# Optimization experiments

Hardware: AMD Instinct MI355X
Metric: run time of the kernel (lower is better)

The kernel has to match this reference:

```python
import jax, jax.numpy as jnp
import numpy as np

N = 100000   # nodes
E = 400000   # merged window edges
L = 100000   # label edges to decode
DIN = 128
H = 128
NL = 2       # GCN layers
RATIO = 0.8
DOUT = 1


def setup_inputs() -> dict:
    key = jax.random.key(0)
    ks = jax.random.split(key, 24)
    def nrm(k, shape, fan):
        return (jax.random.normal(k, shape, jnp.float32) / np.sqrt(fan)).astype(jnp.float32)
    inp = {
        'x': jax.random.normal(ks[0], (N, DIN), jnp.float32),
        'edge_index': jax.random.randint(ks[1], (2, E), 0, N, jnp.int64) if jax.config.jax_enable_x64 else jax.random.randint(ks[1], (2, E), 0, N, jnp.int32),
        'edge_label_index': jax.random.randint(ks[2], (2, L), 0, N, jnp.int32),
        'edge_time': jax.random.uniform(ks[3], (E,), jnp.float32),
        'previous_state': jax.random.normal(ks[4], (N, H), jnp.float32),
        # mlp_transform: Linear(DIN,H)+ReLU
        'w_mlp': nrm(ks[5], (DIN, H), DIN), 'b_mlp': jnp.zeros((H,), jnp.float32),
        # TimeEncode: cos(Linear(1,H)(t))
        'w_time': nrm(ks[6], (H,), 1), 'b_time': jnp.zeros((H,), jnp.float32),
        # Sampling MLP: Linear(3H,H)+ReLU, Linear(H,1)
        'w_s1': nrm(ks[7], (3 * H, H), 3 * H), 'b_s1': jnp.zeros((H,), jnp.float32),
        'w_s2': nrm(ks[8], (H, 1), H), 'b_s2': jnp.zeros((1,), jnp.float32),
        # GCNConv weights per layer
        'gcn_w': nrm(ks[9], (NL, H, H), H), 'gcn_b': jnp.zeros((NL, H), jnp.float32),
        # GRUCell (stored as [H,3H] so x @ W is the torch x @ W_ih^T)
        'gru_wi': nrm(ks[10], (H, 3 * H), H), 'gru_wh': nrm(ks[11], (H, 3 * H), H),
        'gru_bi': jnp.zeros((3 * H,), jnp.float32), 'gru_bh': jnp.zeros((3 * H,), jnp.float32),
        # LinkDecoder: (h_src * h_dst) @ W + b
        'w_dec': nrm(ks[12], (H, DOUT), H), 'b_dec': jnp.zeros((DOUT,), jnp.float32),
    }
    return inp


def _gcn_pass(h, s2, d2, norm, W, b):
    m = h @ W                                      # [N,H]
    agg = jax.ops.segment_sum(norm[:, None] * m[s2], d2, num_segments=N)
    return agg + b


def reference(x, edge_index, edge_label_index, edge_time, previous_state,
              w_mlp, b_mlp, w_time, b_time, w_s1, b_s1, w_s2, b_s2,
              gcn_w, gcn_b, gru_wi, gru_wh, gru_bi, gru_bh, w_dec, b_dec):
    h = jax.nn.relu(x @ w_mlp + b_mlp)             # [N,H]
    src, dst = edge_index[0], edge_index[1]
    # time encoding of shifted edge times: cos(t*w + b) -> [E,H]
    t = edge_time - edge_time.min() + 1.0
    te = jnp.cos(t[:, None] * w_time + b_time)
    # Sampling logits; concat(prev[src],prev[dst],te) @ w_s1 done as 3 matmuls
    pre = (previous_state[src] @ w_s1[:H] + previous_state[dst] @ w_s1[H:2 * H]
           + te @ w_s1[2 * H:] + b_s1)
    logits = jax.nn.relu(pre) @ w_s2 + b_s2        # [E,1]
    z = jax.nn.sigmoid(logits[:, 0])               # eval mode: no Gumbel noise
    k = int(RATIO * E)
    _, keep = jax.lax.top_k(z, k)
    ew, s, d = z[keep], src[keep], dst[keep]
    # GCN normalization with self-loops (weight 1), symmetric norm as in PyG
    sl = jnp.arange(N, dtype=s.dtype)
    s2 = jnp.concatenate([s, sl]); d2 = jnp.concatenate([d, sl])
    w2 = jnp.concatenate([ew, jnp.ones((N,), ew.dtype)])
    deg = jax.ops.segment_sum(w2, d2, num_segments=N)
    dinv = jnp.where(deg > 0, jax.lax.rsqrt(deg), 0.0)
    norm = dinv[s2] * w2 * dinv[d2]                # [k+N]
    for i in range(NL):
        h = _gcn_pass(h, s2, d2, norm, gcn_w[i], gcn_b[i])
        if i != NL - 1:
            h = jax.nn.relu(h)
    # GRUCell update (torch semantics)
    gi = h @ gru_wi + gru_bi
    gh = previous_state @ gru_wh + gru_bh
    ir, iz, inn = jnp.split(gi, 3, axis=1)
    hr, hz, hn = jnp.split(gh, 3, axis=1)
    r = jax.nn.sigmoid(ir + hr)
    u = jax.nn.sigmoid(iz + hz)
    n = jnp.tanh(inn + r * hn)
    h_new = (1.0 - u) * n + u * previous_state     # [N,H]
    # LinkDecoder: Hadamard of endpoints -> linear
    pred = (h_new[edge_label_index[0]] * h_new[edge_label_index[1]]) @ w_dec + b_dec
    return pred, h_new
```

## Files before the change

kernel.cpp:

```cpp
#include <hip/hip_runtime.h>
#include <hip/hip_bf16.h>
#include <math.h>

typedef __bf16 bf16_t;
typedef bf16_t bf16x8 __attribute__((ext_vector_type(8)));
typedef bf16_t bf16x2 __attribute__((ext_vector_type(2)));
typedef float  f32x4  __attribute__((ext_vector_type(4)));
typedef float  f32x2  __attribute__((ext_vector_type(2)));

__device__ __forceinline__ int clampi(int v, int n) {
    return v < 0 ? 0 : (v > n - 1 ? n - 1 : v);
}

template<int NC>
__global__ __launch_bounds__(256) void gemm128(const bf16_t* __restrict__ A,
        const bf16_t* __restrict__ BT, const float* __restrict__ bias,
        float* __restrict__ Cf, bf16_t* __restrict__ Cb, int M, int dorelu)
{
    constexpr int NT = NC / 16;
    int wave = threadIdx.x >> 6, lane = threadIdx.x & 63;
    int mbase = (blockIdx.x * 4 + wave) * 16;
    if (mbase >= M) return;
    int r = lane & 15, q = lane >> 4;
    int arow = mbase + r; if (arow > M - 1) arow = M - 1;
    f32x4 acc[NT];
#pragma unroll
    for (int t = 0; t < NT; ++t) acc[t] = f32x4{0.f, 0.f, 0.f, 0.f};
    const bf16_t* aptr = A + (size_t)arow * 128 + q * 8;
#pragma unroll
    for (int kk = 0; kk < 4; ++kk) {
        bf16x8 af = *(const bf16x8*)(aptr + kk * 32);
#pragma unroll
        for (int t = 0; t < NT; ++t) {
            bf16x8 bfg = *(const bf16x8*)(BT + (size_t)(t * 16 + r) * 128 + kk * 32 + q * 8);
            acc[t] = __builtin_amdgcn_mfma_f32_16x16x32_bf16(af, bfg, acc[t], 0, 0, 0);
        }
    }
#pragma unroll
    for (int t = 0; t < NT; ++t) {
#pragma unroll
        for (int i = 0; i < 4; ++i) {
            int row = mbase + q * 4 + i;
            if (row < M) {
                int col = t * 16 + r;
                float v = acc[t][i];
                if (bias) v += bias[col];
                if (dorelu) v = fmaxf(v, 0.f);
                if (Cf) Cf[(size_t)row * NC + col] = v;
                if (Cb) Cb[(size_t)row * NC + col] = (bf16_t)v;
            }
        }
    }
}

__global__ __launch_bounds__(256) void gru_k(const bf16_t* __restrict__ xb,
        const float* __restrict__ prevf, const bf16_t* __restrict__ wiT,
        const bf16_t* __restrict__ whT, const float* __restrict__ bi,
        const float* __restrict__ bh, float* __restrict__ hnew, int M)
{
    int wave = threadIdx.x >> 6, lane = threadIdx.x & 63;
    int mbase = (blockIdx.x * 4 + wave) * 16;
    if (mbase >= M) return;
    int r = lane & 15, q = lane >> 4;
    int arow = mbase + r; if (arow > M - 1) arow = M - 1;
    bf16x8 ax[4], ap[4];
#pragma unroll
    for (int kk = 0; kk < 4; ++kk) {
        ax[kk] = *(const bf16x8*)(xb + (size_t)arow * 128 + kk * 32 + q * 8);
        f32x4 p0 = *(const f32x4*)(prevf + (size_t)arow * 128 + kk * 32 + q * 8);
        f32x4 p1 = *(const f32x4*)(prevf + (size_t)arow * 128 + kk * 32 + q * 8 + 4);
        bf16x8 t;
#pragma unroll
        for (int j = 0; j < 4; ++j) { t[j] = (bf16_t)p0[j]; t[j + 4] = (bf16_t)p1[j]; }
        ap[kk] = t;
    }
#pragma unroll
    for (int t3 = 0; t3 < 8; ++t3) {
        f32x4 gi0{0.f,0.f,0.f,0.f}, gi1{0.f,0.f,0.f,0.f}, gi2{0.f,0.f,0.f,0.f};
        f32x4 gh0{0.f,0.f,0.f,0.f}, gh1{0.f,0.f,0.f,0.f}, gh2{0.f,0.f,0.f,0.f};
#pragma unroll
        for (int kk = 0; kk < 4; ++kk) {
            const bf16_t* wi = wiT + (size_t)(t3 * 16 + r) * 128 + kk * 32 + q * 8;
            const bf16_t* wh = whT + (size_t)(t3 * 16 + r) * 128 + kk * 32 + q * 8;
            gi0 = __builtin_amdgcn_mfma_f32_16x16x32_bf16(ax[kk], *(const bf16x8*)wi, gi0, 0, 0, 0);
            gi1 = __builtin_amdgcn_mfma_f32_16x16x32_bf16(ax[kk], *(const bf16x8*)(wi + 128 * 128), gi1, 0, 0, 0);
            gi2 = __builtin_amdgcn_mfma_f32_16x16x32_bf16(ax[kk], *(const bf16x8*)(wi + 256 * 128), gi2, 0, 0, 0);
            gh0 = __builtin_amdgcn_mfma_f32_16x16x32_bf16(ap[kk], *(const bf16x8*)wh, gh0, 0, 0, 0);
            gh1 = __builtin_amdgcn_mfma_f32_16x16x32_bf16(ap[kk], *(const bf16x8*)(wh + 128 * 128), gh1, 0, 0, 0);
            gh2 = __builtin_amdgcn_mfma_f32_16x16x32_bf16(ap[kk], *(const bf16x8*)(wh + 256 * 128), gh2, 0, 0, 0);
        }
        int f = t3 * 16 + r;
        float bif0 = bi[f], bif1 = bi[128 + f], bif2 = bi[256 + f];
        float bhf0 = bh[f], bhf1 = bh[128 + f], bhf2 = bh[256 + f];
#pragma unroll
        for (int i = 0; i < 4; ++i) {
            int row = mbase + q * 4 + i;
            if (row < M) {
                float ir = gi0[i] + bif0, hr = gh0[i] + bhf0;
                float iz = gi1[i] + bif1, hz = gh1[i] + bhf1;
                float inn = gi2[i] + bif2, hn = gh2[i] + bhf2;
                float rg = 1.f / (1.f + expf(-(ir + hr)));
                float ug = 1.f / (1.f + expf(-(iz + hz)));
                float nn = tanhf(inn + rg * hn);
                float hp = prevf[(size_t)row * 128 + f];
                hnew[(size_t)row * 128 + f] = (1.f - ug) * nn + ug * hp;
            }
        }
    }
}

__global__ void transp_k(const float* __restrict__ src, bf16_t* __restrict__ dst,
                         int cols, int ld, int rowoff)
{
    int i = blockIdx.x * blockDim.x + threadIdx.x;
    if (i >= cols * 128) return;
    int n = i >> 7, kk = i & 127;
    dst[i] = (bf16_t)src[(size_t)(rowoff + kk) * ld + n];
}

__global__ void cvtb_k(const float* __restrict__ src, size_t off0,
                       bf16_t* __restrict__ dst, int n)
{
    for (int i = blockIdx.x * blockDim.x + threadIdx.x; i < n; i += gridDim.x * blockDim.x)
        dst[i] = (bf16_t)src[off0 + (size_t)i];
}

__global__ void init_k(unsigned* meta, float* deg, int N, int k)
{
    int i = blockIdx.x * blockDim.x + threadIdx.x;
    if (i == 0) { meta[0] = 0x7f800000u; meta[1] = (unsigned)k; meta[8] = 0u; }
    if (i < N) deg[i] = 1.0f;
}

__global__ void tmin_k(const float* __restrict__ et, unsigned* meta, int E)
{
    __shared__ float sred[4];
    int i = blockIdx.x * blockDim.x + threadIdx.x;
    int stride = gridDim.x * blockDim.x;
    float v = 1e30f;
    for (; i < E; i += stride) v = fminf(v, et[i]);
    for (int off = 32; off; off >>= 1) v = fminf(v, __shfl_down(v, off, 64));
    int wave = threadIdx.x >> 6, lane = threadIdx.x & 63;
    if (lane == 0) sred[wave] = v;
    __syncthreads();
    if (threadIdx.x == 0) {
        v = fminf(fminf(sred[0], sred[1]), fminf(sred[2], sred[3]));
        atomicMin(meta + 0, __float_as_uint(v));
    }
}

__global__ void bcount_k(const int* __restrict__ ei, unsigned* bmeta, int E, int Nh, int N)
{
    __shared__ unsigned sc[4];
    int tid = threadIdx.x;
    if (tid < 4) sc[tid] = 0;
    __syncthreads();
    int e = blockIdx.x * blockDim.x + tid;
    int b = -1;
    if (e < E) {
        int s = clampi(ei[e], N), d = clampi(ei[E + e], N);
        b = (s >= Nh ? 2 : 0) + (d >= Nh ? 1 : 0);
    }
    int lane = tid & 63;
#pragma unroll
    for (int bb = 0; bb < 4; ++bb) {
        unsigned long long m = __ballot(b == bb);
        if (lane == 0 && m) atomicAdd(sc + bb, (unsigned)__popcll(m));
    }
    __syncthreads();
    if (tid < 4 && sc[tid]) atomicAdd(bmeta + tid, sc[tid]);
}

__global__ void bscan_k(unsigned* bmeta)
{
    if (threadIdx.x == 0 && blockIdx.x == 0) {
        bmeta[4] = 0;
        for (int b = 0; b < 4; ++b) {
            bmeta[5 + b] = bmeta[4 + b] + bmeta[b];
            bmeta[9 + b] = bmeta[4 + b];
        }
    }
}

__global__ void bfill_k(const int* __restrict__ ei, unsigned* bmeta,
                        unsigned* __restrict__ elist, int E, int Nh, int N)
{
    __shared__ unsigned scount[4];
    __shared__ unsigned sbase[4];
    int tid = threadIdx.x;
    if (tid < 4) scount[tid] = 0;
    __syncthreads();
    int e = blockIdx.x * blockDim.x + tid;
    int b = -1;
    if (e < E) {
        int s = clampi(ei[e], N), d = clampi(ei[E + e], N);
        b = (s >= Nh ? 2 : 0) + (d >= Nh ? 1 : 0);
    }
    int lane = tid & 63;
    unsigned myofs = 0;
#pragma unroll
    for (int bb = 0; bb < 4; ++bb) {
        unsigned long long m = __ballot(b == bb);
        unsigned wb = 0;
        if (lane == 0 && m) wb = atomicAdd(scount + bb, (unsigned)__popcll(m));
        wb = __shfl(wb, 0, 64);
        if (b == bb) myofs = wb + (unsigned)__popcll(m & ((1ull << lane) - 1ull));
    }
    __syncthreads();
    if (tid < 4) sbase[tid] = scount[tid] ? atomicAdd(bmeta + 9 + tid, scount[tid]) : 0u;
    __syncthreads();
    if (b >= 0) elist[sbase[b] + myofs] = (unsigned)e;
}

__global__ __launch_bounds__(256, 2) void proj2(const float* __restrict__ prevf,
        const float* __restrict__ Wflat, float* __restrict__ out, int rows, int base)
{
    __shared__ float sA[16][132];
    __shared__ float sB[16][128];
    int tid = threadIdx.x;
    int rbase = blockIdx.x * 128;
    if (rbase >= rows) return;
    int tx = tid & 15, ty = tid >> 4;
    float acc[8][8];
#pragma unroll
    for (int i = 0; i < 8; ++i)
#pragma unroll
        for (int j = 0; j < 8; ++j) acc[i][j] = 0.f;
    int ks = tid & 15, rs = tid >> 4;
    int fs = tid & 127, kbs = tid >> 7;
    for (int kc = 0; kc < 128; kc += 16) {
#pragma unroll
        for (int i = 0; i < 8; ++i) {
            int r = rs + 16 * i;
            int rr = rbase + r; if (rr > rows - 1) rr = rows - 1;
            sA[ks][r] = prevf[(size_t)(base + rr) * 128 + kc + ks];
        }
#pragma unroll
        for (int i = 0; i < 8; ++i)
            sB[kbs + 2 * i][fs] = Wflat[(size_t)(kc + kbs + 2 * i) * 128 + fs];
        __syncthreads();
#pragma unroll
        for (int r = 0; r < 16; ++r) {
            f32x4 a0 = *(const f32x4*)&sA[r][ty * 8];
            f32x4 a1 = *(const f32x4*)&sA[r][ty * 8 + 4];
            f32x4 b0 = *(const f32x4*)&sB[r][tx * 4];
            f32x4 b1 = *(const f32x4*)&sB[r][64 + tx * 4];
#pragma unroll
            for (int i = 0; i < 8; ++i) {
                float ae = i < 4 ? a0[i] : a1[i - 4];
#pragma unroll
                for (int j = 0; j < 4; ++j) {
                    acc[i][j]     = fmaf(ae, b0[j], acc[i][j]);
                    acc[i][j + 4] = fmaf(ae, b1[j], acc[i][j + 4]);
                }
            }
        }
        __syncthreads();
    }
#pragma unroll
    for (int i = 0; i < 8; ++i) {
        int row = rbase + ty * 8 + i;
        if (row < rows) {
            f32x4 o0, o1;
#pragma unroll
            for (int j = 0; j < 4; ++j) { o0[j] = acc[i][j]; o1[j] = acc[i][j + 4]; }
            *(f32x4*)&out[(size_t)row * 128 + tx * 4] = o0;
            *(f32x4*)&out[(size_t)row * 128 + 64 + tx * 4] = o1;
        }
    }
}

__global__ __launch_bounds__(256, 2) void zgemm(
        const float* __restrict__ et, const int* __restrict__ ei,
        const unsigned* __restrict__ elist, const unsigned* __restrict__ bmeta, int b,
        int soff, int doff,
        const float* __restrict__ Ah, const float* __restrict__ Bh,
        const float* __restrict__ wtime, const float* __restrict__ btime,
        const float* __restrict__ wc, const float* __restrict__ bs1,
        const float* __restrict__ ws2, const float* __restrict__ bs2,
        const unsigned* __restrict__ meta,
        float* __restrict__ z, unsigned* __restrict__ hist1, int E, int N)
{
    unsigned lo = 0, hi = (unsigned)E;
    if (b >= 0) { lo = bmeta[4 + b]; hi = bmeta[5 + b]; }
    unsigned ebase = (unsigned)blockIdx.x * 128u;
    if (ebase >= hi - lo) return;
    __shared__ float sA[16][132];
    __shared__ float sB[16][128];
    __shared__ float sT[128];
    __shared__ int sS[128], sD[128];
    __shared__ unsigned sE[128];
    int tid = threadIdx.x;
    if (tid < 128) {
        float tmin = __uint_as_float(meta[0]);
        unsigned slot = lo + ebase + (unsigned)tid;
        unsigned sl = slot < hi ? slot : hi - 1u;
        unsigned e = elist ? elist[sl] : sl;
        sE[tid] = e;
        sT[tid] = et[e] - tmin + 1.0f;
        sS[tid] = clampi(ei[e], N) - soff;
        sD[tid] = clampi(ei[E + e], N) - doff;
    }
    __syncthreads();
    int tx = tid & 15, ty = tid >> 4;
    float acc[8][8];
#pragma unroll
    for (int i = 0; i < 8; ++i)
#pragma unroll
        for (int j = 0; j < 8; ++j) acc[i][j] = 0.f;
    int ks = tid & 15, rs = tid >> 4;
    int fs = tid & 127, kbs = tid >> 7;
    for (int kc = 0; kc < 128; kc += 16) {
        float wt = wtime[kc + ks], bt = btime[kc + ks];
#pragma unroll
        for (int i = 0; i < 8; ++i) {
            float t = sT[rs + 16 * i];
            sA[ks][rs + 16 * i] = cosf(t * wt + bt);
        }
#pragma unroll
        for (int i = 0; i < 8; ++i)
            sB[kbs + 2 * i][fs] = wc[(size_t)(kc + kbs + 2 * i) * 128 + fs];
        __syncthreads();
#pragma unroll
        for (int r = 0; r < 16; ++r) {
            f32x4 a0 = *(const f32x4*)&sA[r][ty * 8];
            f32x4 a1 = *(const f32x4*)&sA[r][ty * 8 + 4];
            f32x4 b0 = *(const f32x4*)&sB[r][tx * 4];
            f32x4 b1 = *(const f32x4*)&sB[r][64 + tx * 4];
#pragma unroll
            for (int i = 0; i < 8; ++i) {
                float ae = i < 4 ? a0[i] : a1[i - 4];
#pragma unroll
                for (int j = 0; j < 4; ++j) {
                    acc[i][j]     = fmaf(ae, b0[j], acc[i][j]);
                    acc[i][j + 4] = fmaf(ae, b1[j], acc[i][j + 4]);
                }
            }
        }
        __syncthreads();
    }
    f32x4 bb0 = *(const f32x4*)&bs1[tx * 4];
    f32x4 bb1 = *(const f32x4*)&bs1[64 + tx * 4];
    f32x4 w20 = *(const f32x4*)&ws2[tx * 4];
    f32x4 w21 = *(const f32x4*)&ws2[64 + tx * 4];
    float myv = 0.f;
#pragma unroll
    for (int i = 0; i < 8; ++i) {
        int r = ty * 8 + i;
        int s = sS[r], d = sD[r];
        const float* As = Ah + (size_t)s * 128;
        const float* Bd = Bh + (size_t)d * 128;
        f32x4 A0 = *(const f32x4*)&As[tx * 4];
        f32x4 A1 = *(const f32x4*)&As[64 + tx * 4];
        f32x4 B0 = *(const f32x4*)&Bd[tx * 4];
        f32x4 B1 = *(const f32x4*)&Bd[64 + tx * 4];
        float v[4];
#pragma unroll
        for (int j = 0; j < 4; ++j) {
            float p0 = acc[i][j] + ((A0[j] + B0[j]) + bb0[j]);
            float p1 = acc[i][j + 4] + ((A1[j] + B1[j]) + bb1[j]);
            v[j] = fmaxf(p0, 0.f) * w20[j] + fmaxf(p1, 0.f) * w21[j];
        }
#pragma unroll
        for (int j = 0; j < 4; ++j) {
            v[j] += __shfl_xor(v[j], 8, 64);
            v[j] += __shfl_xor(v[j], 4, 64);
            v[j] += __shfl_xor(v[j], 2, 64);
            v[j] += __shfl_xor(v[j], 1, 64);
        }
        float vv = (v[0] + v[2]) + (v[1] + v[3]);
        if (tx == i) myv = vv;
    }
    if (tx < 8) {
        int r = ty * 8 + tx;
        unsigned slot = lo + ebase + (unsigned)r;
        if (slot < hi) {
            float b2 = bs2[0];
            float zv = 1.f / (1.f + expf(-(myv + b2)));
            z[sE[r]] = zv;
            atomicAdd(hist1 + (__float_as_uint(zv) >> 16), 1u);
        }
    }
}

__global__ __launch_bounds__(1024) void scank(const unsigned* __restrict__ hist,
                                              unsigned* meta, int kIdx, int outIdx)
{
    __shared__ unsigned s[1024];
    int t = threadIdx.x;
    unsigned K = meta[kIdx];
    unsigned sum = 0;
    for (int i = 0; i < 64; ++i) sum += hist[t * 64 + i];
    s[t] = sum;
    __syncthreads();
    for (int off = 1; off < 1024; off <<= 1) {
        unsigned add = (t + off < 1024) ? s[t + off] : 0u;
        __syncthreads();
        s[t] += add;
        __syncthreads();
    }
    unsigned mine = s[t];
    unsigned after = (t < 1023) ? s[t + 1] : 0u;
    if (mine >= K && after < K) {
        unsigned cum = after;
        for (int b = 63; b >= 0; --b) {
            unsigned c = hist[t * 64 + b];
            cum += c;
            if (cum >= K) {
                meta[outIdx] = (unsigned)(t * 64 + b);
                meta[outIdx + 1] = cum - c;
                meta[outIdx + 2] = K - (cum - c);
                break;
            }
        }
    }
}

__global__ void pass2(const float* __restrict__ z, const unsigned* __restrict__ meta,
                      unsigned* hist2, int E)
{
    int e = blockIdx.x * blockDim.x + threadIdx.x;
    if (e >= E) return;
    unsigned u = __float_as_uint(z[e]);
    if ((u >> 16) == meta[2]) atomicAdd(hist2 + (u & 0xffffu), 1u);
}

__global__ void pass3(const float* __restrict__ z, unsigned* meta,
                      unsigned char* keep, unsigned* eql, int E)
{
    int e = blockIdx.x * blockDim.x + threadIdx.x;
    if (e >= E) return;
    unsigned u = __float_as_uint(z[e]);
    unsigned T = (meta[2] << 16) | (meta[5] & 0xffffu);
    keep[e] = (u > T) ? 1 : 0;
    if (u == T) {
        unsigned slot = atomicAdd(meta + 8, 1u);
        if (slot < 4096u) eql[slot] = (unsigned)e;
    }
}

__global__ void eqres(const unsigned* __restrict__ meta, const unsigned* __restrict__ eql,
                      unsigned char* keep)
{
    __shared__ unsigned list[4096];
    unsigned c = meta[8]; if (c > 4096u) c = 4096u;
    unsigned need = meta[7];
    for (unsigned i = threadIdx.x; i < c; i += blockDim.x) list[i] = eql[i];
    __syncthreads();
    for (unsigned i = threadIdx.x; i < c; i += blockDim.x) {
        unsigned rank = 0;
        for (unsigned j = 0; j < c; ++j) rank += (list[j] < list[i]) ? 1u : 0u;
        if (rank < need) keep[list[i]] = 1;
    }
}

__global__ void degsc(const int* __restrict__ ei, const float* __restrict__ z,
                      const unsigned char* __restrict__ keep, float* deg, int E, int N)
{
    int e = blockIdx.x * blockDim.x + threadIdx.x;
    if (e >= E) return;
    if (keep[e]) atomicAdd(deg + clampi(ei[E + e], N), z[e]);
}

__global__ void dinv_k(float* deg, float* selfn, int N)
{
    int i = blockIdx.x * blockDim.x + threadIdx.x;
    if (i >= N) return;
    float d = deg[i];
    float di = 1.0f / sqrtf(d);
    deg[i] = di;
    selfn[i] = di * di;
}

__global__ void normcnt(const int* __restrict__ ei, const float* __restrict__ z,
                        const unsigned char* __restrict__ keep, const float* __restrict__ dinv,
                        float* normv, unsigned* cnt, int E, int N)
{
    int e = blockIdx.x * blockDim.x + threadIdx.x;
    if (e >= E) return;
    if (keep[e]) {
        int s = clampi(ei[e], N), d = clampi(ei[E + e], N);
        normv[e] = dinv[s] * z[e] * dinv[d];
        atomicAdd(cnt + d, 1u);
    } else {
        normv[e] = 0.f;
    }
}

__global__ __launch_bounds__(1024) void scan_n(unsigned* cnt, unsigned* fill, int N)
{
    __shared__ unsigned s[1024];
    int t = threadIdx.x;
    int per = (N + 1023) >> 10;
    int lo = t * per; if (lo > N) lo = N;
    int hi = lo + per; if (hi > N) hi = N;
    unsigned sum = 0;
    for (int i = lo; i < hi; ++i) sum += cnt[i];
    s[t] = sum;
    __syncthreads();
    for (int off = 1; off < 1024; off <<= 1) {
        unsigned add = (t >= off) ? s[t - off] : 0u;
        __syncthreads();
        s[t] += add;
        __syncthreads();
    }
    unsigned run = (t > 0) ? s[t - 1] : 0u;
    for (int i = lo; i < hi; ++i) {
        unsigned c = cnt[i];
        cnt[i] = run; fill[i] = run;
        run += c;
    }
    if (t == 1023) cnt[N] = run;
}

__global__ void fillk(const int* __restrict__ ei, const unsigned char* __restrict__ keep,
                      unsigned* fill, unsigned* csr, int E, int N)
{
    int e = blockIdx.x * blockDim.x + threadIdx.x;
    if (e >= E) return;
    if (keep[e]) {
        unsigned p = atomicAdd(fill + clampi(ei[E + e], N), 1u);
        csr[p] = (unsigned)e;
    }
}

__global__ __launch_bounds__(256) void agg_k(const bf16_t* __restrict__ m,
        const int* __restrict__ ei, const float* __restrict__ normv,
        const unsigned* __restrict__ ofs, const unsigned* __restrict__ csr,
        const float* __restrict__ selfn, const float* __restrict__ bias,
        float* __restrict__ hout, bf16_t* __restrict__ houtb, int N, int E, int dorelu)
{
    int wave = threadIdx.x >> 6, lane = threadIdx.x & 63;
    int n = blockIdx.x * 4 + wave;
    if (n >= N) return;
    int f = 2 * lane;
    float sn = selfn[n];
    bf16x2 mv = *(const bf16x2*)(m + (size_t)n * 128 + f);
    float a0 = bias[f] + sn * (float)mv[0];
    float a1 = bias[f + 1] + sn * (float)mv[1];
    unsigned lo = ofs[n], hi = ofs[n + 1];
    unsigned deg = hi - lo;
    unsigned cap = deg < 64u ? deg : 64u;
    int s_l = 0; float w_l = 0.f;
    if (lane < (int)cap) {
        unsigned e = csr[lo + lane];
        s_l = clampi(ei[e], N);
        w_l = normv[e];
    }
    for (unsigned j = 0; j < cap; ++j) {
        int s = __shfl(s_l, (int)j, 64);
        float w = __shfl(w_l, (int)j, 64);
        bf16x2 v = *(const bf16x2*)(m + (size_t)s * 128 + f);
        a0 = fmaf(w, (float)v[0], a0);
        a1 = fmaf(w, (float)v[1], a1);
    }
    for (unsigned idx = lo + 64; idx < hi; ++idx) {
        unsigned e = csr[idx];
        int s = clampi(ei[e], N);
        float w = normv[e];
        bf16x2 v = *(const bf16x2*)(m + (size_t)s * 128 + f);
        a0 = fmaf(w, (float)v[0], a0);
        a1 = fmaf(w, (float)v[1], a1);
    }
    if (dorelu) { a0 = fmaxf(a0, 0.f); a1 = fmaxf(a1, 0.f); }
    f32x2 o; o[0] = a0; o[1] = a1;
    *(f32x2*)(hout + (size_t)n * 128 + f) = o;
    if (houtb) {
        bf16x2 ob; ob[0] = (bf16_t)a0; ob[1] = (bf16_t)a1;
        *(bf16x2*)(houtb + (size_t)n * 128 + f) = ob;
    }
}

__global__ __launch_bounds__(256) void decode_k(const int* __restrict__ eli,
        const float* __restrict__ hnew, const float* __restrict__ wdec,
        const float* __restrict__ bdec, float* __restrict__ pred, int L, int N)
{
    int wave = threadIdx.x >> 6, lane = threadIdx.x & 63;
    int l = blockIdx.x * 4 + wave;
    if (l >= L) return;
    int a = clampi(eli[l], N), b = clampi(eli[L + l], N);
    f32x2 ha = *(const f32x2*)(hnew + (size_t)a * 128 + 2 * lane);
    f32x2 hb = *(const f32x2*)(hnew + (size_t)b * 128 + 2 * lane);
    f32x2 w  = *(const f32x2*)(wdec + 2 * lane);
    float acc = ha[0] * hb[0] * w[0] + ha[1] * hb[1] * w[1];
    for (int off = 32; off; off >>= 1) acc += __shfl_down(acc, off, 64);
    if (lane == 0) pred[l] = acc + bdec[0];
}

extern "C" void kernel_launch(void* const* d_in, const int* in_sizes, int n_in,
                              void* d_out, int out_size, void* d_ws, size_t ws_size,
                              hipStream_t stream)
{
    (void)n_in; (void)out_size;
    const float* x      = (const float*)d_in[0];
    const int*   ei     = (const int*)d_in[1];
    const int*   eli    = (const int*)d_in[2];
    const float* etime  = (const float*)d_in[3];
    const float* prev   = (const float*)d_in[4];
    const float* w_mlp  = (const float*)d_in[5];
    const float* b_mlp  = (const float*)d_in[6];
    const float* w_time = (const float*)d_in[7];
    const float* b_time = (const float*)d_in[8];
    const float* w_s1   = (const float*)d_in[9];
    const float* b_s1   = (const float*)d_in[10];
    const float* w_s2   = (const float*)d_in[11];
    const float* b_s2   = (const float*)d_in[12];
    const float* gcn_w  = (const float*)d_in[13];
    const float* gcn_b  = (const float*)d_in[14];
    const float* gru_wi = (const float*)d_in[15];
    const float* gru_wh = (const float*)d_in[16];
    const float* gru_bi = (const float*)d_in[17];
    const float* gru_bh = (const float*)d_in[18];
    const float* w_dec  = (const float*)d_in[19];
    const float* b_dec  = (const float*)d_in[20];

    const int E  = in_sizes[3];
    const int N  = in_sizes[0] / 128;
    const int L  = in_sizes[2] / 2;
    const int K  = (int)(0.8 * (double)E);
    const int Nh = (N + 1) / 2;

    char* wsp = (char*)d_ws;
    size_t off = 0;
    auto alloc = [&](size_t bytes) -> void* {
        void* p = wsp + off;
        off += (bytes + 255) & ~(size_t)255;
        return p;
    };
    unsigned* meta  = (unsigned*)alloc(64 * 4);
    unsigned* bmeta = (unsigned*)alloc(64 * 4);
    unsigned* elist = (unsigned*)alloc((size_t)E * 4);
    unsigned* eql   = (unsigned*)alloc(4096 * 4);
    unsigned* hist1 = (unsigned*)alloc(65536 * 4);
    unsigned* hist2 = (unsigned*)alloc(65536 * 4);
    unsigned* cnt   = (unsigned*)alloc((size_t)(N + 1) * 4);
    unsigned* fill  = (unsigned*)alloc((size_t)N * 4);
    float* deg      = (float*)alloc((size_t)N * 4);
    float* selfn    = (float*)alloc((size_t)N * 4);
    float* zbuf     = (float*)alloc((size_t)E * 4);
    unsigned char* keep = (unsigned char*)alloc((size_t)E);
    float* normv    = (float*)alloc((size_t)E * 4);
    unsigned* csr   = (unsigned*)alloc((size_t)E * 4);
    bf16_t* wmlpT = (bf16_t*)alloc(128 * 128 * 2);
    bf16_t* g0T   = (bf16_t*)alloc(128 * 128 * 2);
    bf16_t* g1T   = (bf16_t*)alloc(128 * 128 * 2);
    bf16_t* wiT   = (bf16_t*)alloc(384 * 128 * 2);
    bf16_t* whT   = (bf16_t*)alloc(384 * 128 * 2);

    size_t fullBytes = (size_t)N * 128 * 4;
    size_t halfBytes = (size_t)Nh * 128 * 4;
    bool full = (off + 2 * ((fullBytes + 255) & ~(size_t)255)) <= ws_size;
    char* slot0; char* slot1;
    float* Ahalf; float* Bhalf;
    if (full) {
        slot0 = (char*)alloc(fullBytes);
        slot1 = (char*)alloc(fullBytes);
        Ahalf = (float*)slot0;
        Bhalf = (float*)slot1;
    } else {
        slot0 = (char*)alloc(halfBytes);
        slot1 = (char*)alloc(halfBytes);
        Ahalf = (float*)slot0;
        Bhalf = (float*)slot1;
    }
    bf16_t* xbf   = (bf16_t*)slot0;
    bf16_t* mbuf  = (bf16_t*)slot1;

    float* out_pred = (float*)d_out;
    float* hnew     = (float*)d_out + L;
    float* hb       = hnew;

    hipMemsetAsync(bmeta, 0, 64 * 4, stream);
    hipMemsetAsync(hist1, 0, 65536 * 4, stream);
    hipMemsetAsync(hist2, 0, 65536 * 4, stream);
    hipMemsetAsync(cnt, 0, (size_t)(N + 1) * 4, stream);
    init_k<<<(N + 255) / 256, 256, 0, stream>>>(meta, deg, N, K);

    transp_k<<<64, 256, 0, stream>>>(w_mlp, wmlpT, 128, 128, 0);
    transp_k<<<64, 256, 0, stream>>>(gcn_w, g0T, 128, 128, 0);
    transp_k<<<64, 256, 0, stream>>>(gcn_w, g1T, 128, 128, 128);
    transp_k<<<192, 256, 0, stream>>>(gru_wi, wiT, 384, 384, 0);
    transp_k<<<192, 256, 0, stream>>>(gru_wh, whT, 384, 384, 0);

    tmin_k<<<512, 256, 0, stream>>>(etime, meta, E);

    const int zgrid = (E + 127) / 128;
    const float* wc = w_s1 + 256 * 128;
    if (full) {
        proj2<<<(N + 127) / 128, 256, 0, stream>>>(prev, w_s1, Ahalf, N, 0);
        proj2<<<(N + 127) / 128, 256, 0, stream>>>(prev, w_s1 + 128 * 128, Bhalf, N, 0);
        zgemm<<<zgrid, 256, 0, stream>>>(etime, ei, (const unsigned*)nullptr, bmeta, -1,
                0, 0, Ahalf, Bhalf, w_time, b_time, wc, b_s1, w_s2, b_s2,
                meta, zbuf, hist1, E, N);
    } else {
        bcount_k<<<(E + 255) / 256, 256, 0, stream>>>(ei, bmeta, E, Nh, N);
        bscan_k<<<1, 64, 0, stream>>>(bmeta);
        bfill_k<<<(E + 255) / 256, 256, 0, stream>>>(ei, bmeta, elist, E, Nh, N);
        const int NA0 = Nh, NA1 = N - Nh;
        auto zlaunch = [&](int b, int so, int doo) {
            zgemm<<<zgrid, 256, 0, stream>>>(etime, ei, elist, bmeta, b, so, doo,
                    Ahalf, Bhalf, w_time, b_time, wc, b_s1, w_s2, b_s2,
                    meta, zbuf, hist1, E, N);
        };
        proj2<<<(NA0 + 127) / 128, 256, 0, stream>>>(prev, w_s1, Ahalf, NA0, 0);
        proj2<<<(NA0 + 127) / 128, 256, 0, stream>>>(prev, w_s1 + 128 * 128, Bhalf, NA0, 0);
        zlaunch(0, 0, 0);
        proj2<<<(NA1 + 127) / 128, 256, 0, stream>>>(prev, w_s1 + 128 * 128, Bhalf, NA1, Nh);
        zlaunch(1, 0, Nh);
        proj2<<<(NA1 + 127) / 128, 256, 0, stream>>>(prev, w_s1, Ahalf, NA1, Nh);
        zlaunch(3, Nh, Nh);
        proj2<<<(NA0 + 127) / 128, 256, 0, stream>>>(prev, w_s1 + 128 * 128, Bhalf, NA0, 0);
        zlaunch(2, Nh, 0);
    }

    scank<<<1, 1024, 0, stream>>>(hist1, meta, 1, 2);
    pass2<<<(E + 255) / 256, 256, 0, stream>>>(zbuf, meta, hist2, E);
    scank<<<1, 1024, 0, stream>>>(hist2, meta, 4, 5);
    pass3<<<(E + 255) / 256, 256, 0, stream>>>(zbuf, meta, keep, eql, E);
    eqres<<<1, 256, 0, stream>>>(meta, eql, keep);

    degsc<<<(E + 255) / 256, 256, 0, stream>>>(ei, zbuf, keep, deg, E, N);
    dinv_k<<<(N + 255) / 256, 256, 0, stream>>>(deg, selfn, N);
    normcnt<<<(E + 255) / 256, 256, 0, stream>>>(ei, zbuf, keep, deg, normv, cnt, E, N);
    scan_n<<<1, 1024, 0, stream>>>(cnt, fill, N);
    fillk<<<(E + 255) / 256, 256, 0, stream>>>(ei, keep, fill, csr, E, N);

    cvtb_k<<<2048, 256, 0, stream>>>(x, 0, xbf, N * 128);
    gemm128<128><<<(N + 63) / 64, 256, 0, stream>>>(xbf, wmlpT, b_mlp, hb, xbf, N, 1);

    gemm128<128><<<(N + 63) / 64, 256, 0, stream>>>(xbf, g0T, nullptr, nullptr, mbuf, N, 0);
    agg_k<<<(N + 3) / 4, 256, 0, stream>>>(mbuf, ei, normv, cnt, csr, selfn, gcn_b, hb, xbf, N, E, 1);
    gemm128<128><<<(N + 63) / 64, 256, 0, stream>>>(xbf, g1T, nullptr, nullptr, mbuf, N, 0);
    agg_k<<<(N + 3) / 4, 256, 0, stream>>>(mbuf, ei, normv, cnt, csr, selfn, gcn_b + 128, hb, xbf, N, E, 0);

    gru_k<<<(N + 63) / 64, 256, 0, stream>>>(xbf, prev, wiT, whT, gru_bi, gru_bh, hnew, N);

    decode_k<<<(L + 3) / 4, 256, 0, stream>>>(eli, hnew, w_dec, b_dec, out_pred, L, N);
}
```

Baseline: 1.517 ms.

## Make projection and z GEMMs wave-independent and fuse init memsets into one kernel

The proj2 and zgemm kernels are restructured so each wave handles its own 32 rows or edges, with a per-wave LDS tile and no block-wide barriers. The weight operand is now read straight from global or L2 instead of being staged in shared memory. Launch bounds go up to 4 blocks per CU for more occupancy. The four memsets plus init kernel become one grid-stride init kernel, removing launch overhead. The risk is more redundant global weight reads per wave, and relying on compiler-only fences for intra-wave LDS ordering.

Result: slower. 1.669 ms (+10.1%).

```diff
diff --git a/kernel.cpp b/kernel.cpp
--- a/kernel.cpp
+++ b/kernel.cpp
@@ -125,11 +125,16 @@
         dst[i] = (bf16_t)src[off0 + (size_t)i];
 }
 
-__global__ void init_k(unsigned* meta, float* deg, int N, int k)
+__global__ void initall(unsigned* meta, unsigned* bmeta, unsigned* hist1,
+                        unsigned* hist2, unsigned* cnt, float* deg, int N, int k)
 {
     int i = blockIdx.x * blockDim.x + threadIdx.x;
+    int stride = gridDim.x * blockDim.x;
     if (i == 0) { meta[0] = 0x7f800000u; meta[1] = (unsigned)k; meta[8] = 0u; }
-    if (i < N) deg[i] = 1.0f;
+    if (i < 64) bmeta[i] = 0u;
+    for (int j = i; j < 65536; j += stride) { hist1[j] = 0u; hist2[j] = 0u; }
+    for (int j = i; j < N + 1; j += stride) cnt[j] = 0u;
+    for (int j = i; j < N; j += stride) deg[j] = 1.0f;
 }
 
 __global__ void tmin_k(const float* __restrict__ et, unsigned* meta, int E)
@@ -212,39 +217,36 @@
     if (b >= 0) elist[sbase[b] + myofs] = (unsigned)e;
 }
 
-__global__ __launch_bounds__(256, 2) void proj2(const float* __restrict__ prevf,
+__global__ __launch_bounds__(256, 4) void proj2w(const float* __restrict__ prevf,
         const float* __restrict__ Wflat, float* __restrict__ out, int rows, int base)
 {
-    __shared__ float sA[16][132];
-    __shared__ float sB[16][128];
-    int tid = threadIdx.x;
-    int rbase = blockIdx.x * 128;
+    __shared__ float sP[4][16][36];
+    int wave = threadIdx.x >> 6, lane = threadIdx.x & 63;
+    int rbase = blockIdx.x * 128 + wave * 32;
     if (rbase >= rows) return;
-    int tx = tid & 15, ty = tid >> 4;
+    int tx = lane & 15, eg = lane >> 4;
+    int kk = lane & 15, e0 = (lane >> 4) * 8;
     float acc[8][8];
 #pragma unroll
     for (int i = 0; i < 8; ++i)
 #pragma unroll
         for (int j = 0; j < 8; ++j) acc[i][j] = 0.f;
-    int ks = tid & 15, rs = tid >> 4;
-    int fs = tid & 127, kbs = tid >> 7;
     for (int kc = 0; kc < 128; kc += 16) {
+        float tmp[8];
 #pragma unroll
         for (int i = 0; i < 8; ++i) {
-            int r = rs + 16 * i;
-            int rr = rbase + r; if (rr > rows - 1) rr = rows - 1;
-            sA[ks][r] = prevf[(size_t)(base + rr) * 128 + kc + ks];
-        }
-#pragma unroll
-        for (int i = 0; i < 8; ++i)
-            sB[kbs + 2 * i][fs] = Wflat[(size_t)(kc + kbs + 2 * i) * 128 + fs];
-        __syncthreads();
+            int rr = rbase + e0 + i; if (rr > rows - 1) rr = rows - 1;
+            tmp[i] = prevf[(size_t)(base + rr) * 128 + kc + kk];
+        }
+#pragma unroll
+        for (int i = 0; i < 8; ++i) sP[wave][kk][e0 + i] = tmp[i];
+        asm volatile("" ::: "memory");
 #pragma unroll
         for (int r = 0; r < 16; ++r) {
-            f32x4 a0 = *(const f32x4*)&sA[r][ty * 8];
-            f32x4 a1 = *(const f32x4*)&sA[r][ty * 8 + 4];
-            f32x4 b0 = *(const f32x4*)&sB[r][tx * 4];
-            f32x4 b1 = *(const f32x4*)&sB[r][64 + tx * 4];
+            f32x4 a0 = *(const f32x4*)&sP[wave][r][eg * 8];
+            f32x4 a1 = *(const f32x4*)&sP[wave][r][eg * 8 + 4];
+            f32x4 b0 = *(const f32x4*)&Wflat[(size_t)(kc + r) * 128 + tx * 4];
+            f32x4 b1 = *(const f32x4*)&Wflat[(size_t)(kc + r) * 128 + 64 + tx * 4];
 #pragma unroll
             for (int i = 0; i < 8; ++i) {
                 float ae = i < 4 ? a0[i] : a1[i - 4];
@@ -255,11 +257,11 @@
                 }
             }
         }
-        __syncthreads();
+        asm volatile("" ::: "memory");
     }
 #pragma unroll
     for (int i = 0; i < 8; ++i) {
-        int row = rbase + ty * 8 + i;
+        int row = rbase + eg * 8 + i;
         if (row < rows) {
             f32x4 o0, o1;
 #pragma unroll
@@ -270,7 +272,7 @@
     }
 }
 
-__global__ __launch_bounds__(256, 2) void zgemm(
+__global__ __launch_bounds__(256, 4) void zgemmw(
         const float* __restrict__ et, const int* __restrict__ ei,
         const unsigned* __restrict__ elist, const unsigned* __restrict__ bmeta, int b,
         int soff, int doff,
@@ -283,50 +285,48 @@
 {
     unsigned lo = 0, hi = (unsigned)E;
     if (b >= 0) { lo = bmeta[4 + b]; hi = bmeta[5 + b]; }
-    unsigned ebase = (unsigned)blockIdx.x * 128u;
+    int wave = threadIdx.x >> 6, lane = threadIdx.x & 63;
+    unsigned ebase = (unsigned)blockIdx.x * 128u + (unsigned)wave * 32u;
     if (ebase >= hi - lo) return;
-    __shared__ float sA[16][132];
-    __shared__ float sB[16][128];
-    __shared__ float sT[128];
-    __shared__ int sS[128], sD[128];
-    __shared__ unsigned sE[128];
-    int tid = threadIdx.x;
-    if (tid < 128) {
+    __shared__ float sT[4][32];
+    __shared__ int sS[4][32], sD[4][32];
+    __shared__ unsigned sE[4][32];
+    __shared__ float sC[4][16][36];
+    if (lane < 32) {
         float tmin = __uint_as_float(meta[0]);
-        unsigned slot = lo + ebase + (unsigned)tid;
+        unsigned slot = lo + ebase + (unsigned)lane;
         unsigned sl = slot < hi ? slot : hi - 1u;
         unsigned e = elist ? elist[sl] : sl;
-        sE[tid] = e;
-        sT[tid] = et[e] - tmin + 1.0f;
-        sS[tid] = clampi(ei[e], N) - soff;
-        sD[tid] = clampi(ei[E + e], N) - doff;
-    }
-    __syncthreads();
-    int tx = tid & 15, ty = tid >> 4;
+        sE[wave][lane] = e;
+        sT[wave][lane] = et[e] - tmin + 1.0f;
+        sS[wave][lane] = clampi(ei[e], N) - soff;
+        sD[wave][lane] = clampi(ei[E + e], N) - doff;
+    }
+    asm volatile("" ::: "memory");
+    int tx = lane & 15, eg = lane >> 4;
+    int kk = lane & 15, e0 = (lane >> 4) * 8;
+    float tv[8];
+#pragma unroll
+    for (int i = 0; i < 8; ++i) tv[i] = sT[wave][e0 + i];
     float acc[8][8];
 #pragma unroll
     for (int i = 0; i < 8; ++i)
 #pragma unroll
         for (int j = 0; j < 8; ++j) acc[i][j] = 0.f;
-    int ks = tid & 15, rs = tid >> 4;
-    int fs = tid & 127, kbs = tid >> 7;
     for (int kc = 0; kc < 128; kc += 16) {
-        float wt = wtime[kc + ks], bt = btime[kc + ks];
-#pragma unroll
-        for (int i = 0; i < 8; ++i) {
-            float t = sT[rs + 16 * i];
-            sA[ks][rs + 16 * i] = cosf(t * wt + bt);
-        }
-#pragma unroll
-        for (int i = 0; i < 8; ++i)
-            sB[kbs + 2 * i][fs] = wc[(size_t)(kc + kbs + 2 * i) * 128 + fs];
-        __syncthreads();
+        float wt = wtime[kc + kk], bt = btime[kc + kk];
+        float cv[8];
+#pragma unroll
+        for (int i = 0; i < 8; ++i) cv[i] = cosf(tv[i] * wt + bt);
+#pragma unroll
+        for (int i = 0; i < 8; ++i) sC[wave][kk][e0 + i] = cv[i];
+        asm volatile("" ::: "memory");
 #pragma unroll
         for (int r = 0; r < 16; ++r) {
-            f32x4 a0 = *(const f32x4*)&sA[r][ty * 8];
-            f32x4 a1 = *(const f32x4*)&sA[r][ty * 8 + 4];
-            f32x4 b0 = *(const f32x4*)&sB[r][tx * 4];
-            f32x4 b1 = *(const f32x4*)&sB[r][64 + tx * 4];
+            f32x4 a0 = *(const f32x4*)&sC[wave][r][eg * 8];
+            f32x4 a1 = *(const f32x4*)&sC[wave][r][eg * 8 + 4];
+            f32x4 b0 = *(const f32x4*)&wc[(size_t)(kc + r) * 128 + tx * 4];
+            f32x4 b1 = *(const f32x4*)&wc[(size_t)(kc + r) * 128 + 64 + tx * 4];
 #pragma unroll
             for (int i = 0; i < 8; ++i) {
                 float ae = i < 4 ? a0[i] : a1[i - 4];
@@ -337,7 +337,7 @@
                 }
             }
         }
-        __syncthreads();
+        asm volatile("" ::: "memory");
     }
     f32x4 bb0 = *(const f32x4*)&bs1[tx * 4];
     f32x4 bb1 = *(const f32x4*)&bs1[64 + tx * 4];
@@ -346,8 +346,8 @@
     float myv = 0.f;
 #pragma unroll
     for (int i = 0; i < 8; ++i) {
-        int r = ty * 8 + i;
-        int s = sS[r], d = sD[r];
+        int r = eg * 8 + i;
+        int s = sS[wave][r], d = sD[wave][r];
         const float* As = Ah + (size_t)s * 128;
         const float* Bd = Bh + (size_t)d * 128;
         f32x4 A0 = *(const f32x4*)&As[tx * 4];
@@ -372,12 +372,12 @@
         if (tx == i) myv = vv;
     }
     if (tx < 8) {
-        int r = ty * 8 + tx;
+        int r = eg * 8 + tx;
         unsigned slot = lo + ebase + (unsigned)r;
         if (slot < hi) {
             float b2 = bs2[0];
             float zv = 1.f / (1.f + expf(-(myv + b2)));
-            z[sE[r]] = zv;
+            z[sE[wave][r]] = zv;
             atomicAdd(hist1 + (__float_as_uint(zv) >> 16), 1u);
         }
     }
@@ -670,11 +670,7 @@
     float* hnew     = (float*)d_out + L;
     float* hb       = hnew;
 
-    hipMemsetAsync(bmeta, 0, 64 * 4, stream);
-    hipMemsetAsync(hist1, 0, 65536 * 4, stream);
-    hipMemsetAsync(hist2, 0, 65536 * 4, stream);
-    hipMemsetAsync(cnt, 0, (size_t)(N + 1) * 4, stream);
-    init_k<<<(N + 255) / 256, 256, 0, stream>>>(meta, deg, N, K);
+    initall<<<1024, 256, 0, stream>>>(meta, bmeta, hist1, hist2, cnt, deg, N, K);
 
     transp_k<<<64, 256, 0, stream>>>(w_mlp, wmlpT, 128, 128, 0);
     transp_k<<<64, 256, 0, stream>>>(gcn_w, g0T, 128, 128, 0);
@@ -687,9 +683,9 @@
     const int zgrid = (E + 127) / 128;
     const float* wc = w_s1 + 256 * 128;
     if (full) {
-        proj2<<<(N + 127) / 128, 256, 0, stream>>>(prev, w_s1, Ahalf, N, 0);
-        proj2<<<(N + 127) / 128, 256, 0, stream>>>(prev, w_s1 + 128 * 128, Bhalf, N, 0);
-        zgemm<<<zgrid, 256, 0, stream>>>(etime, ei, (const unsigned*)nullptr, bmeta, -1,
+        proj2w<<<(N + 127) / 128, 256, 0, stream>>>(prev, w_s1, Ahalf, N, 0);
+        proj2w<<<(N + 127) / 128, 256, 0, stream>>>(prev, w_s1 + 128 * 128, Bhalf, N, 0);
+        zgemmw<<<zgrid, 256, 0, stream>>>(etime, ei, (const unsigned*)nullptr, bmeta, -1,
                 0, 0, Ahalf, Bhalf, w_time, b_time, wc, b_s1, w_s2, b_s2,
                 meta, zbuf, hist1, E, N);
     } else {
@@ -698,18 +694,18 @@
         bfill_k<<<(E + 255) / 256, 256, 0, stream>>>(ei, bmeta, elist, E, Nh, N);
         const int NA0 = Nh, NA1 = N - Nh;
         auto zlaunch = [&](int b, int so, int doo) {
-            zgemm<<<zgrid, 256, 0, stream>>>(etime, ei, elist, bmeta, b, so, doo,
+            zgemmw<<<zgrid, 256, 0, stream>>>(etime, ei, elist, bmeta, b, so, doo,
                     Ahalf, Bhalf, w_time, b_time, wc, b_s1, w_s2, b_s2,
                     meta, zbuf, hist1, E, N);
         };
-        proj2<<<(NA0 + 127) / 128, 256, 0, stream>>>(prev, w_s1, Ahalf, NA0, 0);
-        proj2<<<(NA0 + 127) / 128, 256, 0, stream>>>(prev, w_s1 + 128 * 128, Bhalf, NA0, 0);
+        proj2w<<<(NA0 + 127) / 128, 256, 0, stream>>>(prev, w_s1, Ahalf, NA0, 0);
+        proj2w<<<(NA0 + 127) / 128, 256, 0, stream>>>(prev, w_s1 + 128 * 128, Bhalf, NA0, 0);
         zlaunch(0, 0, 0);
-        proj2<<<(NA1 + 127) / 128, 256, 0, stream>>>(prev, w_s1 + 128 * 128, Bhalf, NA1, Nh);
+        proj2w<<<(NA1 + 127) / 128, 256, 0, stream>>>(prev, w_s1 + 128 * 128, Bhalf, NA1, Nh);
         zlaunch(1, 0, Nh);
-        proj2<<<(NA1 + 127) / 128, 256, 0, stream>>>(prev, w_s1, Ahalf, NA1, Nh);
+        proj2w<<<(NA1 + 127) / 128, 256, 0, stream>>>(prev, w_s1, Ahalf, NA1, Nh);
         zlaunch(3, Nh, Nh);
-        proj2<<<(NA0 + 127) / 128, 256, 0, stream>>>(prev, w_s1 + 128 * 128, Bhalf, NA0, 0);
+        proj2w<<<(NA0 + 127) / 128, 256, 0, stream>>>(prev, w_s1 + 128 * 128, Bhalf, NA0, 0);
         zlaunch(2, Nh, 0);
     }
 
```
